# Kernel optimization log

Hardware: AMD Instinct MI355X
Metric: run time of the kernel (lower is better)

The kernel has to match this reference:

```python
import jax, jax.numpy as jnp
import numpy as np

NUM_LAYERS = 8
H = 4096  # input_size == hidden_size == output_size


def setup_inputs() -> dict:
    key = jax.random.key(0)
    ks = jax.random.split(key, 8)
    s_in = 1.0 / np.sqrt(H)  # nn.Linear default init scale
    inp = {
        "x": jax.random.normal(ks[0], (1, H), dtype=jnp.float32),
        # stacked per-layer weights: layer0 input_size == hidden_size == H
        "Wxh": jax.random.uniform(ks[1], (NUM_LAYERS, H, H), jnp.float32, -s_in, s_in),
        "bxh": jax.random.uniform(ks[2], (NUM_LAYERS, H), jnp.float32, -s_in, s_in),
        "Whh": jax.random.uniform(ks[3], (NUM_LAYERS, H, H), jnp.float32, -s_in, s_in),
        "bhh": jax.random.uniform(ks[4], (NUM_LAYERS, H), jnp.float32, -s_in, s_in),
        "fc_w": jax.random.uniform(ks[5], (H, H), jnp.float32, -s_in, s_in),
        "fc_b": jax.random.uniform(ks[6], (H,), jnp.float32, -s_in, s_in),
    }
    return inp


def reference(x, Wxh, bxh, Whh, bhh, fc_w, fc_b):
    # hidden states are freshly zeroed every forward in the original module,
    # so Whh(h) reduces to its bias bhh (Whh weights see only zeros).
    h = x  # [1, H]
    h_zero = jnp.zeros((1, H), dtype=x.dtype)
    for i in range(NUM_LAYERS):
        combined = h @ Wxh[i].T + bxh[i] + h_zero @ Whh[i].T + bhh[i]
        h = jnp.tanh(combined)
    out = h @ fc_w.T + fc_b  # [1, H]
    return out
```

## Files before the change

### kernel.cpp

```cpp
#include <hip/hip_runtime.h>
#include <math.h>

#define H 4096
#define NLAYERS 8

__global__ __launch_bounds__(256) void gemv_bias_act(
    const float* __restrict__ W,
    const float* __restrict__ b1,
    const float* __restrict__ b2,
    const float* __restrict__ x,
    float* __restrict__ y,
    int do_tanh)
{
    __shared__ float sx[H];

    const float4* __restrict__ x4 = (const float4*)x;
    float4* sx4 = (float4*)sx;
#pragma unroll
    for (int i = 0; i < H / 4 / 256; ++i) {
        sx4[threadIdx.x + i * 256] = x4[threadIdx.x + i * 256];
    }
    __syncthreads();

    const int lane = threadIdx.x & 63;
    const int wave = threadIdx.x >> 6;
    const int row  = blockIdx.x * 4 + wave;

    const float4* __restrict__ w4 = (const float4*)(W + (size_t)row * H);

    float acc = 0.f;
#pragma unroll
    for (int it = 0; it < H / (64 * 4); ++it) {
        const int k = it * 64 + lane;
        float4 w = w4[k];
        float4 h = sx4[k];
        acc += w.x * h.x + w.y * h.y + w.z * h.z + w.w * h.w;
    }

#pragma unroll
    for (int off = 32; off > 0; off >>= 1)
        acc += __shfl_down(acc, off, 64);

    if (lane == 0) {
        float v = acc + b1[row];
        if (b2) v += b2[row];
        y[row] = do_tanh ? tanhf(v) : v;
    }
}

extern "C" void kernel_launch(void* const* d_in, const int* in_sizes, int n_in,
                              void* d_out, int out_size, void* d_ws, size_t ws_size,
                              hipStream_t stream) {
    const float* x    = (const float*)d_in[0];
    const float* Wxh  = (const float*)d_in[1];
    const float* bxh  = (const float*)d_in[2];
    const float* bhh  = (const float*)d_in[4];
    const float* fc_w = (const float*)d_in[5];
    const float* fc_b = (const float*)d_in[6];
    float* out = (float*)d_out;

    float* h0 = (float*)d_ws;
    float* h1 = h0 + H;
    float* buf[2] = { h0, h1 };

    const float* cur = x;
    for (int l = 0; l < NLAYERS; ++l) {
        float* dst = buf[l & 1];
        gemv_bias_act<<<H / 4, 256, 0, stream>>>(
            Wxh + (size_t)l * H * H, bxh + (size_t)l * H, bhh + (size_t)l * H,
            cur, dst, 1);
        cur = dst;
    }
    gemv_bias_act<<<H / 4, 256, 0, stream>>>(fc_w, fc_b, nullptr, cur, out, 0);
}
```

Before: 928.3 us.

## Fuse all RNN layers into one cooperative kernel with register weight prefetch

Result: slower. 2.269 ms (+144.5%).

```diff
diff --git a/kernel.cpp b/kernel.cpp
--- a/kernel.cpp
+++ b/kernel.cpp
@@ -1,8 +1,87 @@
 #include <hip/hip_runtime.h>
+#include <hip/hip_cooperative_groups.h>
 #include <math.h>
+
+namespace cg = cooperative_groups;
 
 #define H 4096
 #define NLAYERS 8
+
+__global__ __launch_bounds__(256, 4) void fused_rnn(
+    const float* __restrict__ Wxh,
+    const float* __restrict__ bxh,
+    const float* __restrict__ bhh,
+    const float* __restrict__ fc_w,
+    const float* __restrict__ fc_b,
+    const float* __restrict__ x,
+    float* __restrict__ h0,
+    float* __restrict__ h1,
+    float* __restrict__ out)
+{
+    cg::grid_group grid = cg::this_grid();
+
+    __shared__ float sx[H];
+    float4* sx4 = (float4*)sx;
+
+    const int lane = threadIdx.x & 63;
+    const int wave = threadIdx.x >> 6;
+    const int row  = blockIdx.x * 4 + wave;
+
+    const float4* __restrict__ x4 = (const float4*)x;
+#pragma unroll
+    for (int i = 0; i < H / 4 / 256; ++i)
+        sx4[threadIdx.x + i * 256] = x4[threadIdx.x + i * 256];
+
+    float4 wbuf[16];
+    {
+        const float4* __restrict__ w4 = (const float4*)(Wxh + (size_t)row * H);
+#pragma unroll
+        for (int it = 0; it < 16; ++it)
+            wbuf[it] = w4[it * 64 + lane];
+    }
+
+    __syncthreads();
+
+    float* hbuf[2] = { h0, h1 };
+
+    for (int l = 0; l <= NLAYERS; ++l) {
+        float acc = 0.f;
+#pragma unroll
+        for (int it = 0; it < 16; ++it) {
+            float4 w = wbuf[it];
+            float4 h = sx4[it * 64 + lane];
+            acc += w.x * h.x + w.y * h.y + w.z * h.z + w.w * h.w;
+        }
+
+        if (l < NLAYERS) {
+            const float* __restrict__ Wn =
+                (l == NLAYERS - 1) ? fc_w : (Wxh + (size_t)(l + 1) * H * H);
+            const float4* __restrict__ wn4 = (const float4*)(Wn + (size_t)row * H);
+#pragma unroll
+            for (int it = 0; it < 16; ++it)
+                wbuf[it] = wn4[it * 64 + lane];
+        }
+
+#pragma unroll
+        for (int off = 32; off > 0; off >>= 1)
+            acc += __shfl_down(acc, off, 64);
+
+        if (l == NLAYERS) {
+            if (lane == 0) out[row] = acc + fc_b[row];
+        } else {
+            if (lane == 0) {
+                float v = acc + bxh[(size_t)l * H + row] + bhh[(size_t)l * H + row];
+                hbuf[l & 1][row] = tanhf(v);
+            }
+            grid.sync();
+            const float4* __restrict__ h4 = (const float4*)hbuf[l & 1];
+#pragma unroll
+            for (int i = 0; i < H / 4 / 256; ++i)
+                sx4[threadIdx.x + i * 256] = h4[threadIdx.x + i * 256];
+            __syncthreads();
+        }
+    }
+}
 
 __global__ __launch_bounds__(256) void gemv_bias_act(
     const float* __restrict__ W,
@@ -17,9 +96,8 @@
     const float4* __restrict__ x4 = (const float4*)x;
     float4* sx4 = (float4*)sx;
 #pragma unroll
-    for (int i = 0; i < H / 4 / 256; ++i) {
+    for (int i = 0; i < H / 4 / 256; ++i)
         sx4[threadIdx.x + i * 256] = x4[threadIdx.x + i * 256];
-    }
     __syncthreads();
 
     const int lane = threadIdx.x & 63;
@@ -61,15 +139,24 @@
 
     float* h0 = (float*)d_ws;
     float* h1 = h0 + H;
-    float* buf[2] = { h0, h1 };
 
-    const float* cur = x;
-    for (int l = 0; l < NLAYERS; ++l) {
-        float* dst = buf[l & 1];
-        gemv_bias_act<<<H / 4, 256, 0, stream>>>(
-            Wxh + (size_t)l * H * H, bxh + (size_t)l * H, bhh + (size_t)l * H,
-            cur, dst, 1);
-        cur = dst;
+    void* args[] = {
+        (void*)&Wxh, (void*)&bxh, (void*)&bhh, (void*)&fc_w, (void*)&fc_b,
+        (void*)&x, (void*)&h0, (void*)&h1, (void*)&out
+    };
+    hipError_t err = hipLaunchCooperativeKernel(
+        (const void*)fused_rnn, dim3(H / 4), dim3(256), args, 0, stream);
+
+    if (err != hipSuccess) {
+        float* buf[2] = { h0, h1 };
+        const float* cur = x;
+        for (int l = 0; l < NLAYERS; ++l) {
+            float* dst = buf[l & 1];
+            gemv_bias_act<<<H / 4, 256, 0, stream>>>(
+                Wxh + (size_t)l * H * H, bxh + (size_t)l * H, bhh + (size_t)l * H,
+                cur, dst, 1);
+            cur = dst;
+        }
+        gemv_bias_act<<<H / 4, 256, 0, stream>>>(fc_w, fc_b, nullptr, cur, out, 0);
     }
-    gemv_bias_act<<<H / 4, 256, 0, stream>>>(fc_w, fc_b, nullptr, cur, out, 0);
 }
```
